# Kernel optimization log

Hardware: AMD Instinct MI355X
Metric: run time of the kernel (lower is better)

The kernel has to match this reference:

```python
import jax, jax.numpy as jnp
import numpy as np

VOCAB, EMBED, HIDDEN = 30522, 512, 512
B, T = 32, 64
START_TOKEN = 101  # BERT [CLS]
W_SCALE = 0.05


def setup_inputs() -> dict:
    key = jax.random.key(0)
    ks = jax.random.split(key, 14)
    n = lambda k, shape: (jax.random.normal(k, shape, jnp.float32) * W_SCALE)
    return {
        "fused_features": jax.random.normal(ks[0], (B, HIDDEN), jnp.float32),
        "target_captions": jax.random.randint(ks[1], (B, T), 0, VOCAB, jnp.int32),
        "tf_mask": jax.random.randint(ks[2], (T,), 0, 2, jnp.int32),
        "emb": n(ks[3], (VOCAB, EMBED)),
        "w_ih0": n(ks[4], (4 * HIDDEN, EMBED)),
        "w_hh0": n(ks[5], (4 * HIDDEN, HIDDEN)),
        "b_ih0": n(ks[6], (4 * HIDDEN,)),
        "b_hh0": n(ks[7], (4 * HIDDEN,)),
        "w_ih1": n(ks[8], (4 * HIDDEN, HIDDEN)),
        "w_hh1": n(ks[9], (4 * HIDDEN, HIDDEN)),
        "b_ih1": n(ks[10], (4 * HIDDEN,)),
        "b_hh1": n(ks[11], (4 * HIDDEN,)),
        "fc_w": n(ks[12], (VOCAB, HIDDEN)),
        "fc_b": n(ks[13], (VOCAB,)),
    }


def _lstm_cell(x, h, c, w_ih, w_hh, b):
    # PyTorch gate order: i, f, g, o
    gates = x @ w_ih.T + h @ w_hh.T + b  # [B, 4H]
    i, f, g, o = jnp.split(gates, 4, axis=-1)
    i, f, o = jax.nn.sigmoid(i), jax.nn.sigmoid(f), jax.nn.sigmoid(o)
    g = jnp.tanh(g)
    c_new = f * c + i * g
    h_new = o * jnp.tanh(c_new)
    return h_new, c_new


def reference(fused_features, target_captions, tf_mask, emb,
              w_ih0, w_hh0, b_ih0, b_hh0,
              w_ih1, w_hh1, b_ih1, b_hh1,
              fc_w, fc_b):
    b0 = b_ih0 + b_hh0
    b1 = b_ih1 + b_hh1
    max_len = target_captions.shape[1]
    # teacher-forcing coin per step; last step never teacher-forces (t < max_len-1)
    use_tf = (tf_mask > 0) & (jnp.arange(max_len) < max_len - 1)  # [T]
    # next-token teacher inputs: target[:, t+1] (last column is a dummy, never used)
    next_teacher = jnp.concatenate(
        [target_captions[:, 1:], target_captions[:, -1:]], axis=1)  # [B, T]

    def step(carry, xs):
        tok, h0, c0, h1, c1 = carry
        teach, tf = xs
        x = emb[tok]  # [B, E]
        h0, c0 = _lstm_cell(x, h0, c0, w_ih0, w_hh0, b0)
        h1, c1 = _lstm_cell(h0, h1, c1, w_ih1, w_hh1, b1)
        logits = h1 @ fc_w.T + fc_b  # [B, V]
        nxt = jnp.where(tf, teach, jnp.argmax(logits, axis=-1).astype(tok.dtype))
        return (nxt, h0, c0, h1, c1), logits

    bsz = fused_features.shape[0]
    tok0 = jnp.full((bsz,), START_TOKEN, jnp.int32)
    zeros = jnp.zeros_like(fused_features)
    carry0 = (tok0, fused_features, zeros, fused_features, zeros)
    _, logits_t = jax.lax.scan(step, carry0, (next_teacher.T, use_tf))  # [T, B, V]
    return jnp.transpose(logits_t, (1, 0, 2))  # [B, T, V]
```

## Files before the change

### kernel.cpp

```cpp
#include <hip/hip_runtime.h>
#include <hip/hip_bf16.h>
#include <math.h>

#define TT 64
#define HH 512
#define VV 30522
#define START_TOK 101
#define NTILE 477
#define KCAND 8
#define TPG 16

typedef __attribute__((ext_vector_type(8))) short short8v;
typedef __attribute__((ext_vector_type(4))) float f32x4;

__device__ inline short f2bf(float x) {
    union { float f; unsigned u; } v; v.f = x;
    unsigned r = v.u + 0x7FFFu + ((v.u >> 16) & 1u);
    return (short)(r >> 16);
}
__device__ inline float bf2f(short s) {
    return __uint_as_float(((unsigned)(unsigned short)s) << 16);
}
__device__ inline unsigned long long packkey(float v, int col) {
    unsigned u = __float_as_uint(v);
    unsigned key = (u & 0x80000000u) ? ~u : (u | 0x80000000u);
    return ((unsigned long long)key << 32) | (unsigned)col;
}
__device__ inline float keyval(unsigned long long k) {
    unsigned hi = (unsigned)(k >> 32);
    unsigned bits = (hi & 0x80000000u) ? (hi ^ 0x80000000u) : ~hi;
    return __uint_as_float(bits);
}
__device__ __forceinline__ int swz(int base) {
    return base ^ ((((base >> 10) ^ (base >> 7)) & 7) << 4);
}


__global__ void init_k(float* ws, const float* __restrict__ fused) {
    int i = blockIdx.x * blockDim.x + threadIdx.x;
    if (i < 16384) {
        float f = fused[i];
        ws[16384 + i] = f;
        ws[32768 + 16384 + i] = f;
        ws[65536 + i] = 0.f;
        ws[81920 + i] = 0.f;
    }
    if (i == 0) ((unsigned*)(ws + 100384))[0] = 0u;
}

__global__ __launch_bounds__(256) void prep_k(const float* __restrict__ fc_w,
                                              short* __restrict__ w_hi,
                                              unsigned* __restrict__ wmax) {
    int r = blockIdx.x * 64 + (threadIdx.x >> 2);
    int seg = threadIdx.x & 3;
    if (r >= VV) return;
    const float* wp = fc_w + (size_t)r * HH + seg * 128;
    short* op = w_hi + (size_t)r * HH + seg * 128;
    float ss = 0.f;
#pragma unroll
    for (int c = 0; c < 16; ++c) {
        float4 x0 = *(const float4*)(wp + c * 8);
        float4 x1 = *(const float4*)(wp + c * 8 + 4);
        ss += x0.x*x0.x + x0.y*x0.y + x0.z*x0.z + x0.w*x0.w
            + x1.x*x1.x + x1.y*x1.y + x1.z*x1.z + x1.w*x1.w;
        short8v s;
        s[0]=f2bf(x0.x); s[1]=f2bf(x0.y); s[2]=f2bf(x0.z); s[3]=f2bf(x0.w);
        s[4]=f2bf(x1.x); s[5]=f2bf(x1.y); s[6]=f2bf(x1.z); s[7]=f2bf(x1.w);
        *(short8v*)(op + c * 8) = s;
    }
    ss += __shfl_xor(ss, 1); ss += __shfl_xor(ss, 2);
    if (seg == 0) atomicMax(wmax, __float_as_uint(sqrtf(ss)));
}

__global__ __launch_bounds__(256) void lstm_step(
    int t, int mode,
    const float* __restrict__ xsrc,
    const int* __restrict__ tokbuf,
    const float* __restrict__ hprev,
    float* __restrict__ hout,
    float* __restrict__ cstate,
    const float* __restrict__ w_ih,
    const float* __restrict__ w_hh,
    const float* __restrict__ b_ih,
    const float* __restrict__ b_hh,
    short* __restrict__ h1b16out)
{
    __shared__ float in_lds[32 * 1026];
    __shared__ float red[32 * 64];
    __shared__ float gate[4 * 64];
    __shared__ int tok_lds[32];

    const int tid = threadIdx.x;
    const int j = tid >> 5, b = tid & 31;
    const int u0 = blockIdx.x * 2;

    if (mode == 0 && tid < 32)
        tok_lds[tid] = (t == 0) ? START_TOK : tokbuf[t * 32 + tid];
    __syncthreads();

    for (int i = tid; i < 32 * 128; i += 256) {
        int bb2 = i >> 7, k4 = (i & 127) * 4;
        const float* rp = (mode == 0) ? (xsrc + (size_t)tok_lds[bb2] * 512) : (xsrc + bb2 * 512);
        *(float4*)&in_lds[bb2 * 1026 + k4] = *(const float4*)(rp + k4);
    }
    for (int i = tid; i < 32 * 128; i += 256) {
        int bb2 = i >> 7, k4 = (i & 127) * 4;
        *(float4*)&in_lds[bb2 * 1026 + 512 + k4] = *(const float4*)(hprev + bb2 * 512 + k4);
    }
    __syncthreads();

    float acc[8];
#pragma unroll
    for (int r = 0; r < 8; ++r) acc[r] = 0.f;
    int rowoff[8];
#pragma unroll
    for (int rl = 0; rl < 8; ++rl) {
        int gt = rl >> 1, ul = rl & 1;
        rowoff[rl] = (gt * 512 + u0 + ul) * 512;
    }

#pragma unroll
    for (int p = 0; p < 4; ++p) {
        const int koff = (p & 1) * 256;
        const int lbase = (p < 2) ? 0 : 512;
        const float* wb = (p < 2) ? w_ih : w_hh;
#pragma unroll
        for (int m2 = 0; m2 < 8; ++m2) {
            int kl = j * 32 + m2 * 4;
            float2 x0 = *(const float2*)&in_lds[b * 1026 + lbase + koff + kl];
            float2 x1 = *(const float2*)&in_lds[b * 1026 + lbase + koff + kl + 2];
#pragma unroll
            for (int rl = 0; rl < 8; ++rl) {
                float4 w4 = *(const float4*)(wb + rowoff[rl] + koff + kl);
                acc[rl] += x0.x * w4.x + x0.y * w4.y + x1.x * w4.z + x1.y * w4.w;
            }
        }
    }

#pragma unroll
    for (int rl = 0; rl < 8; ++rl) red[(b * 8 + rl) * 8 + j] = acc[rl];
    __syncthreads();

    {
        int b2 = tid >> 3, r2 = tid & 7;
        float s = 0.f;
#pragma unroll
        for (int jj = 0; jj < 8; ++jj) s += red[(b2 * 8 + r2) * 8 + jj];
        int gt = r2 >> 1, ul = r2 & 1;
        int rg = gt * 512 + u0 + ul;
        s += b_ih[rg] + b_hh[rg];
        gate[gt * 64 + ul * 32 + b2] = s;
    }
    __syncthreads();

    if (tid < 64) {
        int ul = tid >> 5, b3 = tid & 31;
        float gi = gate[0 * 64 + tid];
        float gf = gate[1 * 64 + tid];
        float gg = gate[2 * 64 + tid];
        float go = gate[3 * 64 + tid];
        float si = 1.f / (1.f + expf(-gi));
        float sf = 1.f / (1.f + expf(-gf));
        float so = 1.f / (1.f + expf(-go));
        float tg = tanhf(gg);
        int u = u0 + ul;
        float cold = cstate[b3 * 512 + u];
        float cn = sf * cold + si * tg;
        cstate[b3 * 512 + u] = cn;
        float h = so * tanhf(cn);
        hout[b3 * 512 + u] = h;
        if (h1b16out) h1b16out[b3 * 512 + u] = f2bf(h);
    }
}

__global__ __launch_bounds__(256) void fcarg(
    int t,
    const int* __restrict__ tfm,
    const short* __restrict__ h1b16_t,
    const short* __restrict__ w_hi,
    const float* __restrict__ fc_b,
    unsigned long long* __restrict__ cand,
    float* __restrict__ xnorm_g,
    const unsigned* __restrict__ wmax)
{
    if (tfm[t] > 0) return;

    __shared__ short a_sh[32 * 512];
    __shared__ float res_sh[32 * 68];
    __shared__ float xnorm_sh[32];
    __shared__ float wmax_sh;
    __shared__ int cnt_sh[32];

    const int tid = threadIdx.x;
    const int blk = blockIdx.x;
    const float NEG_INF = -__builtin_inff();

    {
        int row = tid >> 3, seg = tid & 7;
        const short* hp = h1b16_t + row * 512 + seg * 64;
        float ss = 0.f;
#pragma unroll
        for (int c = 0; c < 8; ++c) {
            short8v v = *(const short8v*)(hp + c * 8);
            int kbase = seg * 64 + c * 8;
            *(short8v*)((char*)a_sh + swz(row * 1024 + kbase * 2)) = v;
#pragma unroll
            for (int e = 0; e < 8; ++e) { float f = bf2f(v[e]); ss += f * f; }
        }
        ss += __shfl_xor(ss, 1); ss += __shfl_xor(ss, 2); ss += __shfl_xor(ss, 4);
        if (seg == 0) xnorm_sh[row] = sqrtf(ss);
        if (tid == 0) wmax_sh = __uint_as_float(*wmax);
    }
    __syncthreads();
    if (blk == 0 && tid < 32) xnorm_g[tid] = xnorm_sh[tid];

    const int w = tid >> 6, l = tid & 63;
    const int n0 = blk * 64 + w * 16;
    int bcol = n0 + (l & 15); if (bcol > VV - 1) bcol = VV - 1;
    const short* bp = w_hi + (size_t)bcol * HH + ((l >> 4) * 8);
    const int r0 = (l & 15), r1 = (l & 15) + 16;
    f32x4 acc0 = {0.f, 0.f, 0.f, 0.f}, acc1 = {0.f, 0.f, 0.f, 0.f};
#pragma unroll
    for (int kt = 0; kt < 16; ++kt) {
        int kb = (kt * 32 + (l >> 4) * 8) * 2;
        short8v bfrag = *(const short8v*)(bp + kt * 32);
        short8v a0 = *(const short8v*)((char*)a_sh + swz(r0 * 1024 + kb));
        short8v a1 = *(const short8v*)((char*)a_sh + swz(r1 * 1024 + kb));
        acc0 = __builtin_amdgcn_mfma_f32_16x16x32_bf16(a0, bfrag, acc0, 0, 0, 0);
        acc1 = __builtin_amdgcn_mfma_f32_16x16x32_bf16(a1, bfrag, acc1, 0, 0, 0);
    }

    {
        float bias = fc_b[bcol];
        bool oob = (n0 + (l & 15)) >= VV;
        int cl = w * 16 + (l & 15);
#pragma unroll
        for (int r = 0; r < 4; ++r) {
            int m = (l >> 4) * 4 + r;
            res_sh[m * 68 + cl]        = oob ? NEG_INF : acc0[r] + bias;
            res_sh[(m + 16) * 68 + cl] = oob ? NEG_INF : acc1[r] + bias;
        }
    }
    __syncthreads();

    {
        int row = tid >> 3, sub = tid & 7;
        float bv = NEG_INF; int bc = 0x7FFFFFFF;
        for (int c = 0; c < 8; ++c) {
            float v = res_sh[row * 68 + sub * 8 + c];
            if (v > bv) { bv = v; bc = blk * 64 + sub * 8 + c; }
        }
#pragma unroll
        for (int d = 1; d < 8; d <<= 1) {
            float ov = __shfl_xor(bv, d);
            int oc = __shfl_xor(bc, d);
            if (ov > bv || (ov == bv && oc < bc)) { bv = ov; bc = oc; }
        }
        unsigned long long* slotp = cand + ((size_t)row * NTILE + blk) * KCAND;
        if (sub == 0) { slotp[0] = packkey(bv, bc); cnt_sh[row] = 1; }
        __syncthreads();
        float cthr = bv - xnorm_sh[row] * wmax_sh * (1.0f / 128.0f);
        for (int c = 0; c < 8; ++c) {
            float v = res_sh[row * 68 + sub * 8 + c];
            int col = blk * 64 + sub * 8 + c;
            if (v >= cthr && col != bc) {
                int idx = atomicAdd(&cnt_sh[row], 1);
                if (idx < KCAND) slotp[idx] = packkey(v, col);
            }
        }
        __syncthreads();
        if (sub == 0) {
            int n = cnt_sh[row]; if (n > KCAND) n = KCAND;
            for (int k = n; k < KCAND; ++k) slotp[k] = 0ull;
        }
    }
}

__global__ __launch_bounds__(256) void argmax_k(
    int t,
    const int* __restrict__ target,
    const int* __restrict__ tfm,
    const unsigned long long* __restrict__ cand,
    const float* __restrict__ h1,
    const float* __restrict__ fc_w,
    const float* __restrict__ fc_b,
    const float* __restrict__ xnorm,
    const unsigned* __restrict__ wmax,
    int* __restrict__ tokbuf)
{
    const int r = blockIdx.x, tid = threadIdx.x;
    if (tfm[t] > 0) {
        if (tid == 0) tokbuf[(t + 1) * 32 + r] = target[r * TT + t + 1];
        return;
    }
    __shared__ unsigned long long red[256];
    __shared__ int list[32];
    __shared__ int lcnt;
    const int n = NTILE * KCAND;
    const unsigned long long* cp = cand + (size_t)r * n;

    unsigned long long m = 0ull;
    for (int i = tid; i < n; i += 256) { unsigned long long k = cp[i]; m = (k > m) ? k : m; }
    red[tid] = m; __syncthreads();
    for (int s = 128; s > 0; s >>= 1) {
        if (tid < s) { unsigned long long o = red[tid + s]; if (o > red[tid]) red[tid] = o; }
        __syncthreads();
    }
    float Mv = keyval(red[0]);
    float thr = Mv - xnorm[r] * __uint_as_float(*wmax) * (1.0f / 128.0f);
    if (tid == 0) lcnt = 0;
    __syncthreads();
    for (int i = tid; i < n; i += 256) {
        unsigned long long k = cp[i];
        if (!k) continue;
        float v = keyval(k);
        if (v >= thr) {
            int idx = atomicAdd(&lcnt, 1);
            if (idx < 32) list[idx] = (int)(k & 0xFFFFFFFFull);
        }
    }
    __syncthreads();
    int nc = lcnt < 32 ? lcnt : 32;

    if (tid < 64) {
        float bv = -__builtin_inff(); int bc = 0x7FFFFFFF;
        for (int jc = 0; jc < nc; ++jc) {
            int col = list[jc];
            const float* wp = fc_w + (size_t)col * HH + tid * 8;
            const float* xp = h1 + r * 512 + tid * 8;
            float4 a0 = *(const float4*)wp, a1 = *(const float4*)(wp + 4);
            float4 b0 = *(const float4*)xp, b1 = *(const float4*)(xp + 4);
            float s = a0.x*b0.x + a0.y*b0.y + a0.z*b0.z + a0.w*b0.w
                    + a1.x*b1.x + a1.y*b1.y + a1.z*b1.z + a1.w*b1.w;
#pragma unroll
            for (int d = 1; d < 64; d <<= 1) s += __shfl_xor(s, d);
            s += fc_b[col];
            if (s > bv || (s == bv && col < bc)) { bv = s; bc = col; }
        }
        if (tid == 0) tokbuf[(t + 1) * 32 + r] = bc;
    }
}

__global__ __launch_bounds__(256) void logits_all(
    const short* __restrict__ h1b16,
    const short* __restrict__ w_hi,
    const float* __restrict__ fc_b,
    float* __restrict__ out)
{
    __shared__ short a_sh[32 * 512];
    float* res_sh = (float*)a_sh;
    const int tid = threadIdx.x;
    const int blk = blockIdx.x;
    const int tg  = blockIdx.y;
    const float NEG_INF = -__builtin_inff();

    const int w = tid >> 6, l = tid & 63;
    const int n0 = blk * 64 + w * 16;
    int bcol = n0 + (l & 15); if (bcol > VV - 1) bcol = VV - 1;
    const bool oob = (n0 + (l & 15)) >= VV;
    const float bias = fc_b[bcol];
    const short* bp = w_hi + (size_t)bcol * HH + ((l >> 4) * 8);
    short8v bfr[16];
#pragma unroll
    for (int kt = 0; kt < 16; ++kt) bfr[kt] = *(const short8v*)(bp + kt * 32);

    const int r0 = (l & 15), r1 = (l & 15) + 16;
    const int srow = tid >> 3, sseg = tid & 7;

    for (int ts = 0; ts < TPG; ++ts) {
        const int t = tg * TPG + ts;
        const short* hp = h1b16 + t * 16384 + srow * 512 + sseg * 64;
#pragma unroll
        for (int c = 0; c < 8; ++c) {
            short8v v = *(const short8v*)(hp + c * 8);
            int kbase = sseg * 64 + c * 8;
            *(short8v*)((char*)a_sh + swz(srow * 1024 + kbase * 2)) = v;
        }
        __syncthreads();

        f32x4 acc0 = {0.f,0.f,0.f,0.f}, acc1 = {0.f,0.f,0.f,0.f};
#pragma unroll
        for (int kt = 0; kt < 16; ++kt) {
            int kb = (kt * 32 + (l >> 4) * 8) * 2;
            short8v a0 = *(const short8v*)((char*)a_sh + swz(r0 * 1024 + kb));
            short8v a1 = *(const short8v*)((char*)a_sh + swz(r1 * 1024 + kb));
            acc0 = __builtin_amdgcn_mfma_f32_16x16x32_bf16(a0, bfr[kt], acc0, 0, 0, 0);
            acc1 = __builtin_amdgcn_mfma_f32_16x16x32_bf16(a1, bfr[kt], acc1, 0, 0, 0);
        }
        __syncthreads();
        {
            int cl = w * 16 + (l & 15);
#pragma unroll
            for (int r = 0; r < 4; ++r) {
                int m = (l >> 4) * 4 + r;
                res_sh[m * 68 + cl]        = oob ? NEG_INF : acc0[r] + bias;
                res_sh[(m + 16) * 68 + cl] = oob ? NEG_INF : acc1[r] + bias;
            }
        }
        __syncthreads();
        for (int i = tid; i < 32 * 64; i += 256) {
            int m = i >> 6, cl = i & 63;
            int col = blk * 64 + cl;
            if (col < VV)
                __builtin_nontemporal_store(res_sh[m * 68 + cl],
                                            &out[((size_t)m * TT + t) * VV + col]);
        }
        __syncthreads();
    }
}

extern "C" void kernel_launch(void* const* d_in, const int* in_sizes, int n_in,
                              void* d_out, int out_size, void* d_ws, size_t ws_size,
                              hipStream_t stream) {
    const float* fused  = (const float*)d_in[0];
    const int*   target = (const int*)d_in[1];
    const int*   tfm    = (const int*)d_in[2];
    const float* emb    = (const float*)d_in[3];
    const float* w_ih0  = (const float*)d_in[4];
    const float* w_hh0  = (const float*)d_in[5];
    const float* b_ih0  = (const float*)d_in[6];
    const float* b_hh0  = (const float*)d_in[7];
    const float* w_ih1  = (const float*)d_in[8];
    const float* w_hh1  = (const float*)d_in[9];
    const float* b_ih1  = (const float*)d_in[10];
    const float* b_hh1  = (const float*)d_in[11];
    const float* fc_w   = (const float*)d_in[12];
    const float* fc_b   = (const float*)d_in[13];
    float* out = (float*)d_out;

    float* ws = (float*)d_ws;
    float* h0buf = ws;
    float* h1buf = ws + 32768;
    float* c0 = ws + 65536;
    float* c1 = ws + 81920;
    int* tokbuf = (int*)(ws + 98304);
    float* xnorm = ws + 100352;
    unsigned* wmax = (unsigned*)(ws + 100384);
    unsigned long long* cand = (unsigned long long*)(ws + 100416);
    short* w_hi = (short*)(ws + 344640);
    short* h1b16 = (short*)(ws + 8158272);

    init_k<<<64, 256, 0, stream>>>(ws, fused);
    prep_k<<<NTILE, 256, 0, stream>>>(fc_w, w_hi, wmax);

    for (int t = 0; t < TT; ++t) {
        const float* h0prev = h0buf + ((t + 1) & 1) * 16384;
        float*       h0cur  = h0buf + (t & 1) * 16384;
        const float* h1prev = h1buf + ((t + 1) & 1) * 16384;
        float*       h1cur  = h1buf + (t & 1) * 16384;

        lstm_step<<<256, 256, 0, stream>>>(t, 0, emb, tokbuf,
                                           h0prev, h0cur, c0, w_ih0, w_hh0, b_ih0, b_hh0,
                                           nullptr);
        lstm_step<<<256, 256, 0, stream>>>(t, 1, h0cur, tokbuf,
                                           h1prev, h1cur, c1, w_ih1, w_hh1, b_ih1, b_hh1,
                                           h1b16 + (size_t)t * 16384);
        if (t < TT - 1) {
            fcarg<<<NTILE, 256, 0, stream>>>(t, tfm, h1b16 + (size_t)t * 16384,
                                             w_hi, fc_b, cand, xnorm, wmax);
            argmax_k<<<32, 256, 0, stream>>>(t, target, tfm, cand, h1cur, fc_w, fc_b,
                                             xnorm, wmax, tokbuf);
        }
    }
    logits_all<<<dim3(NTILE, TT / TPG), 256, 0, stream>>>(h1b16, w_hi, fc_b, out);
}
```

Measured before the change: 3.416 ms.

## Fuse argmax refinement into fcarg via last-block-done counter; move teacher-forcing to lstm

The separate argmax_k launch is removed. Each fcarg block now increments a per-step atomic counter, and the last block to finish reduces the candidate lists and does the exact fp32 rescoring for all 32 rows. The teacher-forcing token lookup moves into the layer-0 LSTM kernel, so forced steps no longer need any argmax work. This saves one kernel launch per step, at the cost of serialising the final reduction onto a single block. TPG is also halved, which doubles the grid of the final logits kernel.

```diff
diff --git a/kernel.cpp b/kernel.cpp
--- a/kernel.cpp
+++ b/kernel.cpp
@@ -8,7 +8,7 @@
 #define START_TOK 101
 #define NTILE 477
 #define KCAND 8
-#define TPG 16
+#define TPG 8
 
 typedef __attribute__((ext_vector_type(8))) short short8v;
 typedef __attribute__((ext_vector_type(4))) float f32x4;
@@ -46,6 +46,7 @@
         ws[81920 + i] = 0.f;
     }
     if (i == 0) ((unsigned*)(ws + 100384))[0] = 0u;
+    if (i < 64) ((int*)(ws + 100416))[i] = 0;
 }
 
 __global__ __launch_bounds__(256) void prep_k(const float* __restrict__ fc_w,
@@ -75,6 +76,8 @@
 __global__ __launch_bounds__(256) void lstm_step(
     int t, int mode,
     const float* __restrict__ xsrc,
+    const int* __restrict__ target,
+    const int* __restrict__ tfm,
     const int* __restrict__ tokbuf,
     const float* __restrict__ hprev,
     float* __restrict__ hout,
@@ -94,8 +97,13 @@
     const int j = tid >> 5, b = tid & 31;
     const int u0 = blockIdx.x * 2;
 
-    if (mode == 0 && tid < 32)
-        tok_lds[tid] = (t == 0) ? START_TOK : tokbuf[t * 32 + tid];
+    if (mode == 0 && tid < 32) {
+        int tok;
+        if (t == 0) tok = START_TOK;
+        else if (tfm[t - 1] > 0) tok = target[tid * TT + t];
+        else tok = tokbuf[t * 32 + tid];
+        tok_lds[tid] = tok;
+    }
     __syncthreads();
 
     for (int i = tid; i < 32 * 128; i += 256) {
@@ -177,11 +185,14 @@
     int t,
     const int* __restrict__ tfm,
     const short* __restrict__ h1b16_t,
+    const float* __restrict__ h1,
     const short* __restrict__ w_hi,
+    const float* __restrict__ fc_w,
     const float* __restrict__ fc_b,
     unsigned long long* __restrict__ cand,
-    float* __restrict__ xnorm_g,
-    const unsigned* __restrict__ wmax)
+    const unsigned* __restrict__ wmax,
+    int* __restrict__ tokbuf,
+    int* __restrict__ fccnt)
 {
     if (tfm[t] > 0) return;
 
@@ -190,6 +201,10 @@
     __shared__ float xnorm_sh[32];
     __shared__ float wmax_sh;
     __shared__ int cnt_sh[32];
+    __shared__ int last_sh;
+    __shared__ int list_sh[32][32];
+    __shared__ int lcnt_sh[32];
+    __shared__ unsigned long long mx_sh[32];
 
     const int tid = threadIdx.x;
     const int blk = blockIdx.x;
@@ -212,7 +227,6 @@
         if (tid == 0) wmax_sh = __uint_as_float(*wmax);
     }
     __syncthreads();
-    if (blk == 0 && tid < 32) xnorm_g[tid] = xnorm_sh[tid];
 
     const int w = tid >> 6, l = tid & 63;
     const int n0 = blk * 64 + w * 16;
@@ -274,70 +288,66 @@
             for (int k = n; k < KCAND; ++k) slotp[k] = 0ull;
         }
     }
-}
-
-__global__ __launch_bounds__(256) void argmax_k(
-    int t,
-    const int* __restrict__ target,
-    const int* __restrict__ tfm,
-    const unsigned long long* __restrict__ cand,
-    const float* __restrict__ h1,
-    const float* __restrict__ fc_w,
-    const float* __restrict__ fc_b,
-    const float* __restrict__ xnorm,
-    const unsigned* __restrict__ wmax,
-    int* __restrict__ tokbuf)
-{
-    const int r = blockIdx.x, tid = threadIdx.x;
-    if (tfm[t] > 0) {
-        if (tid == 0) tokbuf[(t + 1) * 32 + r] = target[r * TT + t + 1];
-        return;
-    }
-    __shared__ unsigned long long red[256];
-    __shared__ int list[32];
-    __shared__ int lcnt;
-    const int n = NTILE * KCAND;
-    const unsigned long long* cp = cand + (size_t)r * n;
-
-    unsigned long long m = 0ull;
-    for (int i = tid; i < n; i += 256) { unsigned long long k = cp[i]; m = (k > m) ? k : m; }
-    red[tid] = m; __syncthreads();
-    for (int s = 128; s > 0; s >>= 1) {
-        if (tid < s) { unsigned long long o = red[tid + s]; if (o > red[tid]) red[tid] = o; }
-        __syncthreads();
-    }
-    float Mv = keyval(red[0]);
-    float thr = Mv - xnorm[r] * __uint_as_float(*wmax) * (1.0f / 128.0f);
-    if (tid == 0) lcnt = 0;
-    __syncthreads();
-    for (int i = tid; i < n; i += 256) {
-        unsigned long long k = cp[i];
-        if (!k) continue;
-        float v = keyval(k);
-        if (v >= thr) {
-            int idx = atomicAdd(&lcnt, 1);
-            if (idx < 32) list[idx] = (int)(k & 0xFFFFFFFFull);
-        }
-    }
-    __syncthreads();
-    int nc = lcnt < 32 ? lcnt : 32;
-
-    if (tid < 64) {
-        float bv = -__builtin_inff(); int bc = 0x7FFFFFFF;
-        for (int jc = 0; jc < nc; ++jc) {
-            int col = list[jc];
-            const float* wp = fc_w + (size_t)col * HH + tid * 8;
-            const float* xp = h1 + r * 512 + tid * 8;
-            float4 a0 = *(const float4*)wp, a1 = *(const float4*)(wp + 4);
-            float4 b0 = *(const float4*)xp, b1 = *(const float4*)(xp + 4);
-            float s = a0.x*b0.x + a0.y*b0.y + a0.z*b0.z + a0.w*b0.w
-                    + a1.x*b1.x + a1.y*b1.y + a1.z*b1.z + a1.w*b1.w;
-#pragma unroll
-            for (int d = 1; d < 64; d <<= 1) s += __shfl_xor(s, d);
-            s += fc_b[col];
-            if (s > bv || (s == bv && col < bc)) { bv = s; bc = col; }
-        }
-        if (tid == 0) tokbuf[(t + 1) * 32 + r] = bc;
+
+    __syncthreads();
+    if (tid == 0) {
+        __threadfence();
+        int rk = __hip_atomic_fetch_add(&fccnt[t], 1, __ATOMIC_ACQ_REL, __HIP_MEMORY_SCOPE_AGENT);
+        last_sh = (rk == NTILE - 1) ? 1 : 0;
+    }
+    __syncthreads();
+    if (!last_sh) return;
+    __threadfence();
+
+    const int nall = NTILE * KCAND;
+    {
+        int row = tid >> 3, l8 = tid & 7;
+        const unsigned long long* cp = cand + (size_t)row * nall;
+        unsigned long long m = 0ull;
+        for (int i = l8; i < nall; i += 8) { unsigned long long k = cp[i]; if (k > m) m = k; }
+#pragma unroll
+        for (int d = 1; d < 8; d <<= 1) {
+            unsigned long long o = __shfl_xor(m, d);
+            if (o > m) m = o;
+        }
+        if (l8 == 0) { mx_sh[row] = m; lcnt_sh[row] = 0; }
+    }
+    __syncthreads();
+    {
+        int row = tid >> 3, l8 = tid & 7;
+        const unsigned long long* cp = cand + (size_t)row * nall;
+        float Mv = keyval(mx_sh[row]);
+        float thr = Mv - xnorm_sh[row] * wmax_sh * (1.0f / 128.0f);
+        for (int i = l8; i < nall; i += 8) {
+            unsigned long long k = cp[i];
+            if (!k) continue;
+            if (keyval(k) >= thr) {
+                int idx = atomicAdd(&lcnt_sh[row], 1);
+                if (idx < 32) list_sh[row][idx] = (int)(k & 0xFFFFFFFFull);
+            }
+        }
+    }
+    __syncthreads();
+    {
+        int wv = tid >> 6, ln = tid & 63;
+        for (int r2 = wv * 8; r2 < wv * 8 + 8; ++r2) {
+            int nc = lcnt_sh[r2]; if (nc > 32) nc = 32;
+            float bv = NEG_INF; int bc2 = 0x7FFFFFFF;
+            for (int jc = 0; jc < nc; ++jc) {
+                int col = list_sh[r2][jc];
+                const float* wp = fc_w + (size_t)col * HH + ln * 8;
+                const float* xp = h1 + (size_t)r2 * 512 + ln * 8;
+                float4 a0 = *(const float4*)wp, a1 = *(const float4*)(wp + 4);
+                float4 b0 = *(const float4*)xp, b1 = *(const float4*)(xp + 4);
+                float s = a0.x*b0.x + a0.y*b0.y + a0.z*b0.z + a0.w*b0.w
+                        + a1.x*b1.x + a1.y*b1.y + a1.z*b1.z + a1.w*b1.w;
+#pragma unroll
+                for (int d = 1; d < 64; d <<= 1) s += __shfl_xor(s, d);
+                s += fc_b[col];
+                if (s > bv || (s == bv && col < bc2)) { bv = s; bc2 = col; }
+            }
+            if (ln == 0) tokbuf[(t + 1) * 32 + r2] = bc2;
+        }
     }
 }
 
@@ -434,11 +444,11 @@
     float* c0 = ws + 65536;
     float* c1 = ws + 81920;
     int* tokbuf = (int*)(ws + 98304);
-    float* xnorm = ws + 100352;
     unsigned* wmax = (unsigned*)(ws + 100384);
-    unsigned long long* cand = (unsigned long long*)(ws + 100416);
-    short* w_hi = (short*)(ws + 344640);
-    short* h1b16 = (short*)(ws + 8158272);
+    int* fccnt = (int*)(ws + 100416);
+    unsigned long long* cand = (unsigned long long*)(ws + 100480);
+    short* w_hi = (short*)(ws + 344704);
+    short* h1b16 = (short*)(ws + 8158336);
 
     init_k<<<64, 256, 0, stream>>>(ws, fused);
     prep_k<<<NTILE, 256, 0, stream>>>(fc_w, w_hi, wmax);
@@ -449,18 +459,15 @@
         const float* h1prev = h1buf + ((t + 1) & 1) * 16384;
         float*       h1cur  = h1buf + (t & 1) * 16384;
 
-        lstm_step<<<256, 256, 0, stream>>>(t, 0, emb, tokbuf,
+        lstm_step<<<256, 256, 0, stream>>>(t, 0, emb, target, tfm, tokbuf,
                                            h0prev, h0cur, c0, w_ih0, w_hh0, b_ih0, b_hh0,
                                            nullptr);
-        lstm_step<<<256, 256, 0, stream>>>(t, 1, h0cur, tokbuf,
+        lstm_step<<<256, 256, 0, stream>>>(t, 1, h0cur, target, tfm, tokbuf,
                                            h1prev, h1cur, c1, w_ih1, w_hh1, b_ih1, b_hh1,
                                            h1b16 + (size_t)t * 16384);
-        if (t < TT - 1) {
-            fcarg<<<NTILE, 256, 0, stream>>>(t, tfm, h1b16 + (size_t)t * 16384,
-                                             w_hi, fc_b, cand, xnorm, wmax);
-            argmax_k<<<32, 256, 0, stream>>>(t, target, tfm, cand, h1cur, fc_w, fc_b,
-                                             xnorm, wmax, tokbuf);
-        }
+        if (t < TT - 1)
+            fcarg<<<NTILE, 256, 0, stream>>>(t, tfm, h1b16 + (size_t)t * 16384, h1cur,
+                                             w_hi, fc_w, fc_b, cand, wmax, tokbuf, fccnt);
     }
     logits_all<<<dim3(NTILE, TT / TPG), 256, 0, stream>>>(h1b16, w_hi, fc_b, out);
 }
```

Measured after the change: 10.92 ms. +219.6%, slower.
